# Performance work log

Measured on AMD Instinct MI355X. Metric: run time of the kernel, lower is better.

## Reference

```python
import jax, jax.numpy as jnp
import numpy as np

N = 100_000   # nodes
E = 1_600_000 # edges (avg degree 16)
D = 128       # input_dim
H = 128       # hidden_dim
G = 64        # graphs in batch
C = 2         # num_classes


def setup_inputs() -> dict:
    key = jax.random.key(0)
    ks = jax.random.split(key, 16)
    x = jax.random.normal(ks[0], (N, D), dtype=jnp.float32)
    edge_index = jax.random.randint(ks[1], (2, E), 0, N, dtype=jnp.int32)
    batch = jnp.sort(jax.random.randint(ks[2], (N,), 0, G, dtype=jnp.int32))
    def lin(k, fin, fout):
        s = 1.0 / np.sqrt(fin)
        kw, kb = jax.random.split(k)
        W = jax.random.uniform(kw, (fin, fout), jnp.float32, -s, s)
        b = jax.random.uniform(kb, (fout,), jnp.float32, -s, s)
        return W, b
    W0, b0 = lin(ks[3], D, H)
    W1, b1 = lin(ks[4], H, H)
    W2, b2 = lin(ks[5], H, H)
    Wc1, bc1 = lin(ks[6], 2 * H, H)
    Wc2, bc2 = lin(ks[7], H, C)
    return dict(x=x, edge_index=edge_index, batch=batch,
                W0=W0, b0=b0, W1=W1, b1=b1, W2=W2, b2=b2,
                Wc1=Wc1, bc1=bc1, Wc2=Wc2, bc2=bc2)


def _gcn_layer(x, W, b, src, dst, dinv):
    # GCNConv with self-loops and symmetric normalization:
    # out_i = sum_{j->i} d_j^{-1/2} d_i^{-1/2} (x_j W) + d_i^{-1} (x_i W) + b
    h = x @ W                                   # [N, H]
    coef = dinv[src] * dinv[dst]                # [E]
    agg = jax.ops.segment_sum(h[src] * coef[:, None], dst, num_segments=N)
    return agg + h * (dinv * dinv)[:, None] + b


def reference(x, edge_index, batch, W0, b0, W1, b1, W2, b2, Wc1, bc1, Wc2, bc2):
    src, dst = edge_index[0], edge_index[1]
    # degree with self-loops (in-degree on target nodes + 1)
    deg = jax.ops.segment_sum(jnp.ones((E,), jnp.float32), dst, num_segments=N) + 1.0
    dinv = jax.lax.rsqrt(deg)
    for W, b in ((W0, b0), (W1, b1), (W2, b2)):
        x = jax.nn.relu(_gcn_layer(x, W, b, src, dst, dinv))
        # dropout: inference mode -> identity
    # global mean pool per graph
    sums = jax.ops.segment_sum(x, batch, num_segments=G)            # [G, H]
    cnt = jax.ops.segment_sum(jnp.ones((N,), jnp.float32), batch, num_segments=G)
    pooled = sums / jnp.maximum(cnt, 1.0)[:, None]
    combined = jnp.concatenate([pooled, pooled], axis=1)            # [G, 2H]
    hcls = jax.nn.relu(combined @ Wc1 + bc1)
    return hcls @ Wc2 + bc2                                         # [G, C]
```

## Files before the change

kernel.cpp:

```cpp
#include <hip/hip_runtime.h>

#define HDIM 128
#define GCOUNT 64
#define CHUNK 2048

__device__ __forceinline__ float bfl(unsigned u) { return __uint_as_float(u << 16); }
__device__ __forceinline__ unsigned short f2bf(float f) {
  unsigned u = __float_as_uint(f);
  unsigned r = (u + 0x7fffu + ((u >> 16) & 1u)) >> 16;
  return (unsigned short)r;
}
__device__ __forceinline__ unsigned pk2(float a, float b) {
  return (unsigned)f2bf(a) | ((unsigned)f2bf(b) << 16);
}

typedef __attribute__((ext_vector_type(8))) short short8;
typedef __attribute__((ext_vector_type(4))) float f32x4;

__device__ __forceinline__ unsigned qb(float v, float rinv) {
  int q = (int)rintf(v * rinv);
  return (unsigned)(q & 0xff);
}


__global__ void mega1(const float* __restrict__ W0, const float* __restrict__ W1,
                      const float* __restrict__ W2,
                      unsigned short* __restrict__ h0, unsigned short* __restrict__ l0,
                      unsigned short* __restrict__ h1, unsigned short* __restrict__ l1,
                      unsigned short* __restrict__ h2, unsigned short* __restrict__ l2,
                      float* __restrict__ pooled, float* __restrict__ gcnt, int pz,
                      const int* __restrict__ dst, int E, int G, int NB1,
                      int* __restrict__ gcount,
                      const float* __restrict__ x, uint2* __restrict__ S,
                      uint2* __restrict__ Sb, float* __restrict__ csaP,
                      float* __restrict__ csbP,
                      float* __restrict__ cs_base, int n) {
  __shared__ int hist[512];
  int b = blockIdx.x, t = threadIdx.x;
  if (b < 192) {
    int w = b >> 6;
    int idx = (b & 63) * 256 + t;
    const float* W = (w == 0) ? W0 : (w == 1) ? W1 : W2;
    unsigned short* hi = (w == 0) ? h0 : (w == 1) ? h1 : h2;
    unsigned short* lo = (w == 0) ? l0 : (w == 1) ? l1 : l2;
    int k = idx >> 7, nn = idx & 127;
    float wv = W[idx];
    unsigned short h = f2bf(wv);
    float hf = __uint_as_float((unsigned)h << 16);
    unsigned short l = f2bf(wv - hf);
    int kb = k >> 5, quad = (k >> 3) & 3, e = k & 7;
    int nt = nn >> 4, m = nn & 15;
    int di = (((kb * 8 + nt) * 64) + quad * 16 + m) * 8 + e;
    hi[di] = h;
    lo[di] = l;
  } else if (b < 192 + pz) {
    int i = (b - 192) * 256 + t;
    if (i < GCOUNT * HDIM) pooled[i] = 0.f;
    else if (i - GCOUNT * HDIM < GCOUNT) gcnt[i - GCOUNT * HDIM] = 0.f;
    if (b == 192) {
      if (t < 16) S[(size_t)n * 16 + t] = make_uint2(0u, 0u);
      else if (t < 32) Sb[(size_t)n * 16 + (t - 16)] = make_uint2(0u, 0u);
      else if (t == 32) csaP[n] = 0.f;
      else if (t == 33) csbP[n] = 0.f;
    }
  } else if (b < 192 + pz + G) {
    int blk = b - 192 - pz;
    for (int i = t; i < NB1; i += 256) hist[i] = 0;
    __syncthreads();
    int base = blk * CHUNK;
    #pragma unroll
    for (int j = 0; j < CHUNK / 256; j++) {
      int e = base + j * 256 + t;
      if (e < E) atomicAdd(&hist[dst[e] >> 8], 1);
    }
    __syncthreads();
    for (int i = t; i < NB1; i += 256) gcount[i * G + blk] = hist[i];
  } else {
    int idx = (b - 192 - pz - G) * 16 + (t >> 4);
    int l = t & 15;
    int ridx = min(idx, n - 1);
    float4 f0 = ((const float4*)x)[(size_t)ridx * 32 + l * 2];
    float4 f1 = ((const float4*)x)[(size_t)ridx * 32 + l * 2 + 1];
    float v0 = f0.x, v1 = f0.y, v2 = f0.z, v3 = f0.w;
    float v4 = f1.x, v5 = f1.y, v6 = f1.z, v7 = f1.w;
    float mx = fmaxf(fmaxf(fmaxf(fabsf(v0), fabsf(v1)), fmaxf(fabsf(v2), fabsf(v3))),
                     fmaxf(fmaxf(fabsf(v4), fabsf(v5)), fmaxf(fabsf(v6), fabsf(v7))));
    mx = fmaxf(mx, __shfl_xor(mx, 1));
    mx = fmaxf(mx, __shfl_xor(mx, 2));
    mx = fmaxf(mx, __shfl_xor(mx, 4));
    mx = fmaxf(mx, __shfl_xor(mx, 8));
    float c = mx * (1.0f / 127.0f);
    float rinv = (mx > 0.f) ? 127.0f / mx : 0.f;
    if (idx < n) {
      unsigned lo = qb(v0, rinv) | (qb(v1, rinv) << 8) | (qb(v2, rinv) << 16) | (qb(v3, rinv) << 24);
      unsigned hi = qb(v4, rinv) | (qb(v5, rinv) << 8) | (qb(v6, rinv) << 16) | (qb(v7, rinv) << 24);
      S[(size_t)idx * 16 + l] = make_uint2(lo, hi);
      if (l == 0) cs_base[idx] = c;
    }
  }
}


__global__ void scanA(int* __restrict__ g, int* __restrict__ bsum, int M) {
  __shared__ int sh[1024];
  int t = threadIdx.x;
  int i = blockIdx.x * 1024 + t;
  int v = (i < M) ? g[i] : 0;
  sh[t] = v;
  __syncthreads();
  for (int off = 1; off < 1024; off <<= 1) {
    int u = (t >= off) ? sh[t - off] : 0;
    __syncthreads();
    sh[t] += u;
    __syncthreads();
  }
  if (i < M) g[i] = sh[t] - v;
  if (t == 1023) bsum[blockIdx.x] = sh[1023];
}

__global__ void scanB(int* __restrict__ g, const int* __restrict__ bsum, int nb, int M) {
  __shared__ int sh[512];
  int t = threadIdx.x;
  if (t < 512) sh[t] = (t < nb) ? bsum[t] : 0;
  __syncthreads();
  for (int off = 1; off < 512; off <<= 1) {
    int u = (t < 512 && t >= off) ? sh[t - off] : 0;
    __syncthreads();
    if (t < 512) sh[t] += u;
    __syncthreads();
  }
  #pragma unroll
  for (int k = 0; k < 2; k++) {
    int i = blockIdx.x * 2048 + k * 1024 + t;
    if (i < M) {
      int j = i >> 10;
      if (j) g[i] += sh[j - 1];
    }
  }
}


__global__ void rs_scatter(const int* __restrict__ src, const int* __restrict__ dst,
                           const int* __restrict__ gscan, int E, int G, int NB1,
                           uint2* __restrict__ sp) {
  __shared__ int run[512];
  int blk = blockIdx.x, t = threadIdx.x;
  for (int i = t; i < NB1; i += 256) run[i] = gscan[i * G + blk];
  __syncthreads();
  int base = blk * CHUNK;
  #pragma unroll
  for (int j = 0; j < CHUNK / 256; j++) {
    int e = base + j * 256 + t;
    if (e < E) {
      int d = dst[e];
      int pos = atomicAdd(&run[d >> 8], 1);
      sp[pos] = make_uint2((unsigned)d, (unsigned)src[e]);
    }
  }
}


__global__ void csr_fine(const uint2* __restrict__ sp, const int* __restrict__ gscan,
                         int E, int G, int NB1,
                         int* __restrict__ rowp, int* __restrict__ rowe,
                         int* __restrict__ colv,
                         float* __restrict__ dinv, const float* __restrict__ cs_base,
                         float* __restrict__ cs, int n) {
  __shared__ int hist[256];
  __shared__ int scn[256];
  __shared__ int run2[256];
  int hb = blockIdx.x, t = threadIdx.x;
  int O = gscan[hb * G];
  int Oe = (hb == NB1 - 1) ? E : gscan[(hb + 1) * G];
  int PO = ((O + 3) & ~3) + hb * 1024;
  if (t < 256) hist[t] = 0;
  __syncthreads();
  for (int e = O + t; e < Oe; e += 512) atomicAdd(&hist[sp[e].x & 255], 1);
  __syncthreads();
  int v = 0, pv = 0;
  if (t < 256) { v = hist[t]; pv = (v + 3) & ~3; scn[t] = pv; }
  __syncthreads();
  for (int off = 1; off < 256; off <<= 1) {
    int u = (t < 256 && t >= off) ? scn[t - off] : 0;
    __syncthreads();
    if (t < 256) scn[t] += u;
    __syncthreads();
  }
  if (t < 256) {
    int st = PO + scn[t] - pv;
    run2[t] = st;
    int d = (hb << 8) + t;
    rowp[d] = st;
    rowe[d] = st + pv;
    for (int i = v; i < pv; i++) colv[st + i] = n;
    if (d < n) {
      float dv = rsqrtf((float)v + 1.0f);
      dinv[d] = dv;
      cs[d] = cs_base[d] * dv;
    }
  }
  __syncthreads();
  for (int e = O + t; e < Oe; e += 512) {
    uint2 p = sp[e];
    int pos = atomicAdd(&run2[p.x & 255], 1);
    colv[pos] = (int)p.y;
  }
}


__device__ __forceinline__ void acc8(uint2 v, float c, float* a) {
  int xx = (int)v.x, yy = (int)v.y;
  a[0] += c * (float)(signed char)(xx);
  a[1] += c * (float)(signed char)(xx >> 8);
  a[2] += c * (float)(signed char)(xx >> 16);
  a[3] += c * (float)(xx >> 24);
  a[4] += c * (float)(signed char)(yy);
  a[5] += c * (float)(signed char)(yy >> 8);
  a[6] += c * (float)(signed char)(yy >> 16);
  a[7] += c * (float)(yy >> 24);
}


__device__ __forceinline__ void agg_phase(
    const uint2* __restrict__ S, const float* __restrict__ cs,
    const float* __restrict__ dinv,
    const int* __restrict__ rowp, const int* __restrict__ rowe,
    const int* __restrict__ col,
    uint4* At, int block0, int t, int n) {
  int grp = t >> 4, gl = t & 15;
  #pragma unroll 1
  for (int k = 0; k < 4; k++) {
    int lrow = grp * 4 + k;
    int g = block0 + lrow;
    uint4 o = make_uint4(0u, 0u, 0u, 0u);
    if (g < n) {
      float a[8];
      {
        uint2 q = S[(size_t)g * 16 + gl];
        float c = cs[g];
        int xx = (int)q.x, yy = (int)q.y;
        a[0] = c * (float)(signed char)(xx);
        a[1] = c * (float)(signed char)(xx >> 8);
        a[2] = c * (float)(signed char)(xx >> 16);
        a[3] = c * (float)(xx >> 24);
        a[4] = c * (float)(signed char)(yy);
        a[5] = c * (float)(signed char)(yy >> 8);
        a[6] = c * (float)(signed char)(yy >> 16);
        a[7] = c * (float)(yy >> 24);
      }
      int e = rowp[g], e1 = rowe[g];
      if (e < e1) {
        int4 ca = *(const int4*)(col + e);
        uint2 q0 = S[(size_t)ca.x * 16 + gl];
        uint2 q1 = S[(size_t)ca.y * 16 + gl];
        uint2 q2 = S[(size_t)ca.z * 16 + gl];
        uint2 q3 = S[(size_t)ca.w * 16 + gl];
        float c0 = cs[ca.x], c1 = cs[ca.y], c2 = cs[ca.z], c3 = cs[ca.w];
        #pragma unroll 1
        for (e += 4; e < e1; e += 4) {
          int4 cn = *(const int4*)(col + e);
          uint2 p0 = S[(size_t)cn.x * 16 + gl];
          uint2 p1 = S[(size_t)cn.y * 16 + gl];
          uint2 p2 = S[(size_t)cn.z * 16 + gl];
          uint2 p3 = S[(size_t)cn.w * 16 + gl];
          float d0 = cs[cn.x], d1 = cs[cn.y], d2 = cs[cn.z], d3 = cs[cn.w];
          acc8(q0, c0, a); acc8(q1, c1, a); acc8(q2, c2, a); acc8(q3, c3, a);
          q0 = p0; q1 = p1; q2 = p2; q3 = p3;
          c0 = d0; c1 = d1; c2 = d2; c3 = d3;
        }
        acc8(q0, c0, a); acc8(q1, c1, a); acc8(q2, c2, a); acc8(q3, c3, a);
      }
      float d = dinv[g];
      o.x = pk2(a[0] * d, a[1] * d);
      o.y = pk2(a[2] * d, a[3] * d);
      o.z = pk2(a[4] * d, a[5] * d);
      o.w = pk2(a[6] * d, a[7] * d);
    }
    At[(gl << 6) + (lrow ^ (gl & 7))] = o;
  }
}

__device__ __forceinline__ void stage16(uint4* Wl, const uint4* __restrict__ WT, int t) {
  #pragma unroll
  for (int i = 0; i < 4; i++) {
    int idx = t + i * 256;
    Wl[idx] = WT[idx];
  }
}

__device__ __forceinline__ void mfma2(const uint4* Wl, const uint4* av, f32x4* acc,
                                      int kbase, int lane) {
  #pragma unroll
  for (int kk = 0; kk < 2; kk++) {
    short8 af = __builtin_bit_cast(short8, av[kbase + kk]);
    #pragma unroll
    for (int nt = 0; nt < 8; nt++) {
      uint4 b = Wl[(kk * 8 + nt) * 64 + lane];
      acc[nt] = __builtin_amdgcn_mfma_f32_16x16x32_bf16(af, __builtin_bit_cast(short8, b), acc[nt], 0, 0, 0);
    }
  }
}

__global__ __launch_bounds__(256, 4) void fused_q8(
    const uint2* __restrict__ S, const float* __restrict__ cs,
    const float* __restrict__ dinv,
    const int* __restrict__ rowp, const int* __restrict__ rowe,
    const int* __restrict__ col,
    const uint4* __restrict__ WThi, const uint4* __restrict__ WTlo,
    const float* __restrict__ bias,
    unsigned char* __restrict__ Sout, float* __restrict__ csout, int n) {
  __shared__ __align__(16) char smem[16384];
  uint4* At = (uint4*)smem;
  uint4* Wl = (uint4*)smem;
  int t = threadIdx.x;
  int lane = t & 63, wv = t >> 6;
  int m = lane & 15, quad = lane >> 4;
  int block0 = blockIdx.x * 64;

  agg_phase(S, cs, dinv, rowp, rowe, col, At, block0, t, n);
  __syncthreads();

  uint4 av[4];
  #pragma unroll
  for (int kb = 0; kb < 4; kb++) {
    int glr = kb * 4 + quad;
    av[kb] = At[(glr << 6) + ((wv * 16 + m) ^ (glr & 7))];
  }
  __syncthreads();

  f32x4 acc[8];
  #pragma unroll
  for (int i = 0; i < 8; i++) acc[i] = (f32x4){0.f, 0.f, 0.f, 0.f};

  stage16(Wl, WThi, t);        __syncthreads();
  mfma2(Wl, av, acc, 0, lane); __syncthreads();
  stage16(Wl, WThi + 1024, t); __syncthreads();
  mfma2(Wl, av, acc, 2, lane); __syncthreads();
  stage16(Wl, WTlo, t);        __syncthreads();
  mfma2(Wl, av, acc, 0, lane); __syncthreads();
  stage16(Wl, WTlo + 1024, t); __syncthreads();
  mfma2(Wl, av, acc, 2, lane); __syncthreads();

  char* stg = smem;
  float* LcA = (float*)(smem + 9216);
  #pragma unroll
  for (int r = 0; r < 4; r++) {
    int lrow = wv * 16 + quad * 4 + r;
    int grow = block0 + lrow;
    float sc = (grow < n) ? dinv[grow] : 0.f;
    float v[8];
    float mx = 0.f;
    #pragma unroll
    for (int nt = 0; nt < 8; nt++) {
      v[nt] = fmaxf(acc[nt][r] + bias[nt * 16 + m], 0.f) * sc;
      mx = fmaxf(mx, v[nt]);
    }
    mx = fmaxf(mx, __shfl_xor(mx, 1));
    mx = fmaxf(mx, __shfl_xor(mx, 2));
    mx = fmaxf(mx, __shfl_xor(mx, 4));
    mx = fmaxf(mx, __shfl_xor(mx, 8));
    float c = mx * (1.0f / 127.0f);
    float rinv = (mx > 0.f) ? 127.0f / mx : 0.f;
    #pragma unroll
    for (int nt = 0; nt < 8; nt++) {
      stg[lrow * 144 + nt * 16 + m] = (char)(int)rintf(v[nt] * rinv);
    }
    if (m == 0) LcA[lrow] = c;
  }
  __syncthreads();
  for (int i = t; i < 512; i += 256) {
    int lrow = i >> 3, seg = i & 7;
    int grow = block0 + lrow;
    if (grow < n)
      ((uint4*)Sout)[(size_t)grow * 8 + seg] = *(const uint4*)&stg[lrow * 144 + seg * 16];
  }
  if (t < 64 && block0 + t < n) csout[block0 + t] = LcA[t];
}

__global__ __launch_bounds__(256, 4) void fused_final(
    const uint2* __restrict__ S, const float* __restrict__ cs,
    const float* __restrict__ dinv,
    const int* __restrict__ rowp, const int* __restrict__ rowe,
    const int* __restrict__ col,
    const uint4* __restrict__ WThi, const uint4* __restrict__ WTlo,
    const float* __restrict__ bias, const int* __restrict__ batch,
    float* __restrict__ pooled, float* __restrict__ gcnt, int n) {
  __shared__ __align__(16) char smem[16384];
  uint4* At = (uint4*)smem;
  uint4* Wl = (uint4*)smem;
  int t = threadIdx.x;
  int lane = t & 63, wv = t >> 6;
  int m = lane & 15, quad = lane >> 4;
  int block0 = blockIdx.x * 64;

  agg_phase(S, cs, dinv, rowp, rowe, col, At, block0, t, n);
  __syncthreads();

  uint4 av[4];
  #pragma unroll
  for (int kb = 0; kb < 4; kb++) {
    int glr = kb * 4 + quad;
    av[kb] = At[(glr << 6) + ((wv * 16 + m) ^ (glr & 7))];
  }
  __syncthreads();

  f32x4 acc[8];
  #pragma unroll
  for (int i = 0; i < 8; i++) acc[i] = (f32x4){0.f, 0.f, 0.f, 0.f};

  stage16(Wl, WThi, t);        __syncthreads();
  mfma2(Wl, av, acc, 0, lane); __syncthreads();
  stage16(Wl, WThi + 1024, t); __syncthreads();
  mfma2(Wl, av, acc, 2, lane); __syncthreads();
  stage16(Wl, WTlo, t);        __syncthreads();
  mfma2(Wl, av, acc, 0, lane); __syncthreads();
  stage16(Wl, WTlo + 1024, t); __syncthreads();
  mfma2(Wl, av, acc, 2, lane); __syncthreads();

  unsigned short* Ls = (unsigned short*)smem;
  #pragma unroll
  for (int r = 0; r < 4; r++) {
    int lrow = wv * 16 + quad * 4 + r;
    #pragma unroll
    for (int nt = 0; nt < 8; nt++) {
      float v = fmaxf(acc[nt][r] + bias[nt * 16 + m], 0.f);
      Ls[lrow * 128 + nt * 16 + m] = f2bf(v);
    }
  }
  __syncthreads();
  if (t < 128) {
    float a2 = 0.f, cl = 0.f;
    int gcur = -1;
    for (int r = 0; r < 64; r++) {
      int grow = block0 + r;
      if (grow >= n) break;
      int gr = batch[grow];
      if (gr != gcur) {
        if (gcur >= 0) {
          atomicAdd(&pooled[gcur * HDIM + t], a2);
          if (t == 0) atomicAdd(&gcnt[gcur], cl);
        }
        a2 = 0.f; cl = 0.f; gcur = gr;
      }
      a2 += bfl((unsigned)Ls[r * 128 + t]);
      cl += 1.f;
    }
    if (gcur >= 0) {
      atomicAdd(&pooled[gcur * HDIM + t], a2);
      if (t == 0) atomicAdd(&gcnt[gcur], cl);
    }
  }
}


__global__ void cls_kernel(const float* __restrict__ pooled, const float* __restrict__ gcnt,
                           const float* __restrict__ Wc1, const float* __restrict__ bc1,
                           const float* __restrict__ Wc2, const float* __restrict__ bc2,
                           float* __restrict__ out) {
  __shared__ float p[HDIM];
  __shared__ float r0s[HDIM], r1s[HDIM];
  int g = blockIdx.x, t = threadIdx.x;
  float c = fmaxf(gcnt[g], 1.0f);
  p[t] = pooled[g * HDIM + t] / c;
  __syncthreads();
  float acc = bc1[t];
  for (int k = 0; k < HDIM; k++) {
    acc += p[k] * (Wc1[k * HDIM + t] + Wc1[(HDIM + k) * HDIM + t]);
  }
  float h = fmaxf(acc, 0.f);
  r0s[t] = h * Wc2[t * 2 + 0];
  r1s[t] = h * Wc2[t * 2 + 1];
  __syncthreads();
  for (int s2 = 64; s2 > 0; s2 >>= 1) {
    if (t < s2) { r0s[t] += r0s[t + s2]; r1s[t] += r1s[t + s2]; }
    __syncthreads();
  }
  if (t == 0) {
    out[g * 2 + 0] = r0s[0] + bc2[0];
    out[g * 2 + 1] = r1s[0] + bc2[1];
  }
}


extern "C" void kernel_launch(void* const* d_in, const int* in_sizes, int n_in,
                              void* d_out, int out_size, void* d_ws, size_t ws_size,
                              hipStream_t stream) {
  const float* x   = (const float*)d_in[0];
  const int*   ei  = (const int*)d_in[1];
  const int*   bat = (const int*)d_in[2];
  const float* W0  = (const float*)d_in[3];
  const float* b0  = (const float*)d_in[4];
  const float* W1  = (const float*)d_in[5];
  const float* b1  = (const float*)d_in[6];
  const float* W2  = (const float*)d_in[7];
  const float* b2  = (const float*)d_in[8];
  const float* Wc1 = (const float*)d_in[9];
  const float* bc1 = (const float*)d_in[10];
  const float* Wc2 = (const float*)d_in[11];
  const float* bc2 = (const float*)d_in[12];
  float* out = (float*)d_out;

  int N = in_sizes[0] / HDIM;
  int E = in_sizes[1] / 2;
  const int* src = ei;
  const int* dst = ei + E;

  int NB1 = (N + 255) >> 8;
  int G = (E + CHUNK - 1) / CHUNK;
  int M = NB1 * G;

  char* ws = (char*)d_ws;
  size_t off = 0;
  auto alloc = [&](size_t bytes) -> void* {
    void* p = (void*)(ws + off);
    off += (bytes + 511) & ~(size_t)511;
    return p;
  };
  unsigned char* Sa = (unsigned char*)alloc((size_t)(N + 1) * HDIM * 2);
  unsigned char* Sb = Sa + (size_t)(N + 1) * HDIM;
  float* csa  = (float*)alloc((size_t)(N + 2) * 4);
  float* csb  = (float*)alloc((size_t)(N + 2) * 4);
  float* cs_base = (float*)alloc((size_t)N * 4);
  float* dinv = (float*)alloc((size_t)N * 4);
  int*   rowp = (int*)alloc((size_t)(NB1 * 256 + 2) * 4);
  int*   rowe = (int*)alloc((size_t)(NB1 * 256 + 2) * 4);
  int*   colv = (int*)alloc((size_t)(E + NB1 * 1024 + 1024) * 4);
  uint2* sp   = (uint2*)alloc((size_t)E * 8);
  float* pooled = (float*)alloc((size_t)GCOUNT * HDIM * 4);
  float* gcnt   = (float*)alloc((size_t)GCOUNT * 4);
  unsigned short* wt_hi[3], *wt_lo[3];
  for (int i = 0; i < 3; i++) {
    wt_hi[i] = (unsigned short*)alloc(HDIM * HDIM * 2);
    wt_lo[i] = (unsigned short*)alloc(HDIM * HDIM * 2);
  }
  int* gcount = (int*)alloc((size_t)(M + 2) * 4);
  int nbM = (M + 1023) / 1024;
  int* bsum = (int*)alloc((size_t)nbM * 4);

  int pz = (GCOUNT * HDIM + GCOUNT + 255) / 256;
  int psb = (N + 15) / 16;
  mega1<<<192 + pz + G + psb, 256, 0, stream>>>(W0, W1, W2,
      wt_hi[0], wt_lo[0], wt_hi[1], wt_lo[1], wt_hi[2], wt_lo[2],
      pooled, gcnt, pz, dst, E, G, NB1, gcount,
      x, (uint2*)Sa, (uint2*)Sb, csa, csb, cs_base, N);

  scanA<<<nbM, 1024, 0, stream>>>(gcount, bsum, M);
  scanB<<<(M + 2047) / 2048, 1024, 0, stream>>>(gcount, bsum, nbM, M);

  rs_scatter<<<G, 256, 0, stream>>>(src, dst, gcount, E, G, NB1, sp);
  csr_fine<<<NB1, 512, 0, stream>>>(sp, gcount, E, G, NB1, rowp, rowe, colv,
      dinv, cs_base, csa, N);

  int fusedBlocks = (N + 63) / 64;

  fused_q8<<<fusedBlocks, 256, 0, stream>>>((const uint2*)Sa, csa, dinv, rowp, rowe, colv,
      (const uint4*)wt_hi[0], (const uint4*)wt_lo[0], b0, Sb, csb, N);

  fused_q8<<<fusedBlocks, 256, 0, stream>>>((const uint2*)Sb, csb, dinv, rowp, rowe, colv,
      (const uint4*)wt_hi[1], (const uint4*)wt_lo[1], b1, Sa, csa, N);

  fused_final<<<fusedBlocks, 256, 0, stream>>>((const uint2*)Sa, csa, dinv, rowp, rowe, colv,
      (const uint4*)wt_hi[2], (const uint4*)wt_lo[2], b2, bat, pooled, gcnt, N);

  cls_kernel<<<GCOUNT, HDIM, 0, stream>>>(pooled, gcnt, Wc1, bc1, Wc2, bc2, out);
}
```

Baseline: 328.7 us.

## Pack CSR scatter entries, enlarge chunk, and pipeline edge loads across rows

Packs the scatter intermediate into a single 32-bit word per edge (24-bit source plus the low 8 bits of the destination), halving that buffer's traffic, and doubles CHUNK for the radix scatter. The aggregation now treats each thread group's four rows as one continuous edge stream, so the software-pipelined gather prefetch carries across row boundaries instead of draining and refilling per row. This relies on the padded contiguity of the CSR layout and on node ids fitting in 24 bits. It also adds a scheduling barrier and extra control flow inside the inner loop.

```diff
diff --git a/kernel.cpp b/kernel.cpp
--- a/kernel.cpp
+++ b/kernel.cpp
@@ -2,7 +2,7 @@
 
 #define HDIM 128
 #define GCOUNT 64
-#define CHUNK 2048
+#define CHUNK 4096
 
 __device__ __forceinline__ float bfl(unsigned u) { return __uint_as_float(u << 16); }
 __device__ __forceinline__ unsigned short f2bf(float f) {
@@ -142,7 +142,7 @@
 
 __global__ void rs_scatter(const int* __restrict__ src, const int* __restrict__ dst,
                            const int* __restrict__ gscan, int E, int G, int NB1,
-                           uint2* __restrict__ sp) {
+                           unsigned* __restrict__ sp) {
   __shared__ int run[512];
   int blk = blockIdx.x, t = threadIdx.x;
   for (int i = t; i < NB1; i += 256) run[i] = gscan[i * G + blk];
@@ -154,13 +154,13 @@
     if (e < E) {
       int d = dst[e];
       int pos = atomicAdd(&run[d >> 8], 1);
-      sp[pos] = make_uint2((unsigned)d, (unsigned)src[e]);
-    }
-  }
-}
-
-
-__global__ void csr_fine(const uint2* __restrict__ sp, const int* __restrict__ gscan,
+      sp[pos] = (unsigned)src[e] | ((unsigned)(d & 255) << 24);
+    }
+  }
+}
+
+
+__global__ void csr_fine(const unsigned* __restrict__ sp, const int* __restrict__ gscan,
                          int E, int G, int NB1,
                          int* __restrict__ rowp, int* __restrict__ rowe,
                          int* __restrict__ colv,
@@ -175,7 +175,7 @@
   int PO = ((O + 3) & ~3) + hb * 1024;
   if (t < 256) hist[t] = 0;
   __syncthreads();
-  for (int e = O + t; e < Oe; e += 512) atomicAdd(&hist[sp[e].x & 255], 1);
+  for (int e = O + t; e < Oe; e += 512) atomicAdd(&hist[sp[e] >> 24], 1);
   __syncthreads();
   int v = 0, pv = 0;
   if (t < 256) { v = hist[t]; pv = (v + 3) & ~3; scn[t] = pv; }
@@ -201,9 +201,9 @@
   }
   __syncthreads();
   for (int e = O + t; e < Oe; e += 512) {
-    uint2 p = sp[e];
-    int pos = atomicAdd(&run2[p.x & 255], 1);
-    colv[pos] = (int)p.y;
+    unsigned p = sp[e];
+    int pos = atomicAdd(&run2[p >> 24], 1);
+    colv[pos] = (int)(p & 0xFFFFFFu);
   }
 }
 
@@ -228,55 +228,80 @@
     const int* __restrict__ col,
     uint4* At, int block0, int t, int n) {
   int grp = t >> 4, gl = t & 15;
-  #pragma unroll 1
-  for (int k = 0; k < 4; k++) {
-    int lrow = grp * 4 + k;
-    int g = block0 + lrow;
+  int g0 = block0 + grp * 4;
+
+  float a[8];
+  int r = 0;
+
+  auto initRow = [&](int g) {
+    if (g < n) {
+      uint2 q = S[(size_t)g * 16 + gl];
+      float c = cs[g];
+      int xx = (int)q.x, yy = (int)q.y;
+      a[0] = c * (float)(signed char)(xx);
+      a[1] = c * (float)(signed char)(xx >> 8);
+      a[2] = c * (float)(signed char)(xx >> 16);
+      a[3] = c * (float)(xx >> 24);
+      a[4] = c * (float)(signed char)(yy);
+      a[5] = c * (float)(signed char)(yy >> 8);
+      a[6] = c * (float)(signed char)(yy >> 16);
+      a[7] = c * (float)(yy >> 24);
+    } else {
+      #pragma unroll
+      for (int i = 0; i < 8; i++) a[i] = 0.f;
+    }
+  };
+  auto finRow = [&](int rr) {
+    int g = g0 + rr;
     uint4 o = make_uint4(0u, 0u, 0u, 0u);
     if (g < n) {
-      float a[8];
-      {
-        uint2 q = S[(size_t)g * 16 + gl];
-        float c = cs[g];
-        int xx = (int)q.x, yy = (int)q.y;
-        a[0] = c * (float)(signed char)(xx);
-        a[1] = c * (float)(signed char)(xx >> 8);
-        a[2] = c * (float)(signed char)(xx >> 16);
-        a[3] = c * (float)(xx >> 24);
-        a[4] = c * (float)(signed char)(yy);
-        a[5] = c * (float)(signed char)(yy >> 8);
-        a[6] = c * (float)(signed char)(yy >> 16);
-        a[7] = c * (float)(yy >> 24);
-      }
-      int e = rowp[g], e1 = rowe[g];
-      if (e < e1) {
-        int4 ca = *(const int4*)(col + e);
-        uint2 q0 = S[(size_t)ca.x * 16 + gl];
-        uint2 q1 = S[(size_t)ca.y * 16 + gl];
-        uint2 q2 = S[(size_t)ca.z * 16 + gl];
-        uint2 q3 = S[(size_t)ca.w * 16 + gl];
-        float c0 = cs[ca.x], c1 = cs[ca.y], c2 = cs[ca.z], c3 = cs[ca.w];
-        #pragma unroll 1
-        for (e += 4; e < e1; e += 4) {
-          int4 cn = *(const int4*)(col + e);
-          uint2 p0 = S[(size_t)cn.x * 16 + gl];
-          uint2 p1 = S[(size_t)cn.y * 16 + gl];
-          uint2 p2 = S[(size_t)cn.z * 16 + gl];
-          uint2 p3 = S[(size_t)cn.w * 16 + gl];
-          float d0 = cs[cn.x], d1 = cs[cn.y], d2 = cs[cn.z], d3 = cs[cn.w];
-          acc8(q0, c0, a); acc8(q1, c1, a); acc8(q2, c2, a); acc8(q3, c3, a);
-          q0 = p0; q1 = p1; q2 = p2; q3 = p3;
-          c0 = d0; c1 = d1; c2 = d2; c3 = d3;
-        }
-        acc8(q0, c0, a); acc8(q1, c1, a); acc8(q2, c2, a); acc8(q3, c3, a);
-      }
       float d = dinv[g];
       o.x = pk2(a[0] * d, a[1] * d);
       o.y = pk2(a[2] * d, a[3] * d);
       o.z = pk2(a[4] * d, a[5] * d);
       o.w = pk2(a[6] * d, a[7] * d);
     }
+    int lrow = grp * 4 + rr;
     At[(gl << 6) + (lrow ^ (gl & 7))] = o;
+  };
+
+  initRow(g0);
+  int cur = rowp[g0];
+  int stop = rowe[g0];
+  int eEnd = rowe[g0 + 3];
+
+  while (cur >= stop && r < 3) { finRow(r); r++; initRow(g0 + r); stop = rowe[g0 + r]; }
+
+  if (cur < eEnd) {
+    int4 ca = *(const int4*)(col + cur);
+    uint2 q0 = S[(size_t)ca.x * 16 + gl];
+    uint2 q1 = S[(size_t)ca.y * 16 + gl];
+    uint2 q2 = S[(size_t)ca.z * 16 + gl];
+    uint2 q3 = S[(size_t)ca.w * 16 + gl];
+    float c0 = cs[ca.x], c1 = cs[ca.y], c2 = cs[ca.z], c3 = cs[ca.w];
+    #pragma unroll 1
+    for (int e = cur + 4; e < eEnd; e += 4) {
+      int4 cn = *(const int4*)(col + e);
+      uint2 p0 = S[(size_t)cn.x * 16 + gl];
+      uint2 p1 = S[(size_t)cn.y * 16 + gl];
+      uint2 p2 = S[(size_t)cn.z * 16 + gl];
+      uint2 p3 = S[(size_t)cn.w * 16 + gl];
+      float d0 = cs[cn.x], d1 = cs[cn.y], d2 = cs[cn.z], d3 = cs[cn.w];
+      __builtin_amdgcn_sched_barrier(0);
+      acc8(q0, c0, a); acc8(q1, c1, a); acc8(q2, c2, a); acc8(q3, c3, a);
+      cur += 4;
+      while (cur >= stop && r < 3) { finRow(r); r++; initRow(g0 + r); stop = rowe[g0 + r]; }
+      q0 = p0; q1 = p1; q2 = p2; q3 = p3;
+      c0 = d0; c1 = d1; c2 = d2; c3 = d3;
+    }
+    acc8(q0, c0, a); acc8(q1, c1, a); acc8(q2, c2, a); acc8(q3, c3, a);
+  }
+  for (;;) {
+    finRow(r);
+    r++;
+    if (r >= 4) break;
+    initRow(g0 + r);
+    stop = rowe[g0 + r];
   }
 }
 
@@ -525,7 +550,7 @@
   int*   rowp = (int*)alloc((size_t)(NB1 * 256 + 2) * 4);
   int*   rowe = (int*)alloc((size_t)(NB1 * 256 + 2) * 4);
   int*   colv = (int*)alloc((size_t)(E + NB1 * 1024 + 1024) * 4);
-  uint2* sp   = (uint2*)alloc((size_t)E * 8);
+  unsigned* sp = (unsigned*)alloc((size_t)E * 4);
   float* pooled = (float*)alloc((size_t)GCOUNT * HDIM * 4);
   float* gcnt   = (float*)alloc((size_t)GCOUNT * 4);
   unsigned short* wt_hi[3], *wt_lo[3];
```

New measurement: 343.0 us. +4.3%, slower.

## Fold scanB into scatter kernels, pack edge pairs into 32 bits, interleave row bounds

Applied to the files above, without the earlier changes.

Drops the scanB kernel: rs_scatter and csr_fine each redo the small block-sum scan in shared memory and add the offset when they read gcount. Scatter records shrink from 8 bytes to 4 by packing the source index with the low 8 bits of the destination in the top byte. rowp and rowe are merged into one int2 array, so the aggregation reads one 8-byte load per row. The aim is to save a launch and cut traffic during CSR construction, at the cost of redundant scans per block and packing that assumes node ids fit in 24 bits.

```diff
diff --git a/kernel.cpp b/kernel.cpp
--- a/kernel.cpp
+++ b/kernel.cpp
@@ -118,64 +118,74 @@
   if (t == 1023) bsum[blockIdx.x] = sh[1023];
 }
 
-__global__ void scanB(int* __restrict__ g, const int* __restrict__ bsum, int nb, int M) {
-  __shared__ int sh[512];
-  int t = threadIdx.x;
-  if (t < 512) sh[t] = (t < nb) ? bsum[t] : 0;
+
+__global__ void rs_scatter(const int* __restrict__ src, const int* __restrict__ dst,
+                           const int* __restrict__ gscan, const int* __restrict__ bsum,
+                           int nb, int E, int G, int NB1,
+                           unsigned* __restrict__ sp) {
+  __shared__ int run[512];
+  __shared__ int sb[512];
+  int blk = blockIdx.x, t = threadIdx.x;
+  sb[t] = (t < nb) ? bsum[t] : 0;
   __syncthreads();
   for (int off = 1; off < 512; off <<= 1) {
-    int u = (t < 512 && t >= off) ? sh[t - off] : 0;
-    __syncthreads();
-    if (t < 512) sh[t] += u;
-    __syncthreads();
-  }
-  #pragma unroll
-  for (int k = 0; k < 2; k++) {
-    int i = blockIdx.x * 2048 + k * 1024 + t;
-    if (i < M) {
-      int j = i >> 10;
-      if (j) g[i] += sh[j - 1];
-    }
-  }
-}
-
-
-__global__ void rs_scatter(const int* __restrict__ src, const int* __restrict__ dst,
-                           const int* __restrict__ gscan, int E, int G, int NB1,
-                           uint2* __restrict__ sp) {
-  __shared__ int run[512];
-  int blk = blockIdx.x, t = threadIdx.x;
-  for (int i = t; i < NB1; i += 256) run[i] = gscan[i * G + blk];
+    int u = (t >= off) ? sb[t - off] : 0;
+    __syncthreads();
+    sb[t] += u;
+    __syncthreads();
+  }
+  for (int i = t; i < NB1; i += 512) {
+    int idx = i * G + blk;
+    int j = idx >> 10;
+    run[i] = gscan[idx] + (j ? sb[j - 1] : 0);
+  }
   __syncthreads();
   int base = blk * CHUNK;
   #pragma unroll
-  for (int j = 0; j < CHUNK / 256; j++) {
-    int e = base + j * 256 + t;
+  for (int j = 0; j < CHUNK / 512; j++) {
+    int e = base + j * 512 + t;
     if (e < E) {
       int d = dst[e];
       int pos = atomicAdd(&run[d >> 8], 1);
-      sp[pos] = make_uint2((unsigned)d, (unsigned)src[e]);
-    }
-  }
-}
-
-
-__global__ void csr_fine(const uint2* __restrict__ sp, const int* __restrict__ gscan,
+      sp[pos] = (unsigned)src[e] | ((unsigned)(d & 255) << 24);
+    }
+  }
+}
+
+
+__global__ void csr_fine(const unsigned* __restrict__ sp, const int* __restrict__ gscan,
+                         const int* __restrict__ bsum, int nb,
                          int E, int G, int NB1,
-                         int* __restrict__ rowp, int* __restrict__ rowe,
-                         int* __restrict__ colv,
+                         int2* __restrict__ rowpe, int* __restrict__ colv,
                          float* __restrict__ dinv, const float* __restrict__ cs_base,
                          float* __restrict__ cs, int n) {
+  __shared__ int sb[512];
   __shared__ int hist[256];
   __shared__ int scn[256];
   __shared__ int run2[256];
   int hb = blockIdx.x, t = threadIdx.x;
-  int O = gscan[hb * G];
-  int Oe = (hb == NB1 - 1) ? E : gscan[(hb + 1) * G];
+  sb[t] = (t < nb) ? bsum[t] : 0;
+  __syncthreads();
+  for (int off = 1; off < 512; off <<= 1) {
+    int u = (t >= off) ? sb[t - off] : 0;
+    __syncthreads();
+    sb[t] += u;
+    __syncthreads();
+  }
+  int iO = hb * G;
+  int jO = iO >> 10;
+  int O = gscan[iO] + (jO ? sb[jO - 1] : 0);
+  int Oe;
+  if (hb == NB1 - 1) Oe = E;
+  else {
+    int i2 = (hb + 1) * G;
+    int j2 = i2 >> 10;
+    Oe = gscan[i2] + (j2 ? sb[j2 - 1] : 0);
+  }
   int PO = ((O + 3) & ~3) + hb * 1024;
   if (t < 256) hist[t] = 0;
   __syncthreads();
-  for (int e = O + t; e < Oe; e += 512) atomicAdd(&hist[sp[e].x & 255], 1);
+  for (int e = O + t; e < Oe; e += 512) atomicAdd(&hist[sp[e] >> 24], 1);
   __syncthreads();
   int v = 0, pv = 0;
   if (t < 256) { v = hist[t]; pv = (v + 3) & ~3; scn[t] = pv; }
@@ -190,8 +200,7 @@
     int st = PO + scn[t] - pv;
     run2[t] = st;
     int d = (hb << 8) + t;
-    rowp[d] = st;
-    rowe[d] = st + pv;
+    rowpe[d] = make_int2(st, st + pv);
     for (int i = v; i < pv; i++) colv[st + i] = n;
     if (d < n) {
       float dv = rsqrtf((float)v + 1.0f);
@@ -201,9 +210,9 @@
   }
   __syncthreads();
   for (int e = O + t; e < Oe; e += 512) {
-    uint2 p = sp[e];
-    int pos = atomicAdd(&run2[p.x & 255], 1);
-    colv[pos] = (int)p.y;
+    unsigned p = sp[e];
+    int pos = atomicAdd(&run2[p >> 24], 1);
+    colv[pos] = (int)(p & 0xFFFFFFu);
   }
 }
 
@@ -224,7 +233,7 @@
 __device__ __forceinline__ void agg_phase(
     const uint2* __restrict__ S, const float* __restrict__ cs,
     const float* __restrict__ dinv,
-    const int* __restrict__ rowp, const int* __restrict__ rowe,
+    const int2* __restrict__ rowpe,
     const int* __restrict__ col,
     uint4* At, int block0, int t, int n) {
   int grp = t >> 4, gl = t & 15;
@@ -248,7 +257,8 @@
         a[6] = c * (float)(signed char)(yy >> 16);
         a[7] = c * (float)(yy >> 24);
       }
-      int e = rowp[g], e1 = rowe[g];
+      int2 pe = rowpe[g];
+      int e = pe.x, e1 = pe.y;
       if (e < e1) {
         int4 ca = *(const int4*)(col + e);
         uint2 q0 = S[(size_t)ca.x * 16 + gl];
@@ -304,7 +314,7 @@
 __global__ __launch_bounds__(256, 4) void fused_q8(
     const uint2* __restrict__ S, const float* __restrict__ cs,
     const float* __restrict__ dinv,
-    const int* __restrict__ rowp, const int* __restrict__ rowe,
+    const int2* __restrict__ rowpe,
     const int* __restrict__ col,
     const uint4* __restrict__ WThi, const uint4* __restrict__ WTlo,
     const float* __restrict__ bias,
@@ -317,7 +327,7 @@
   int m = lane & 15, quad = lane >> 4;
   int block0 = blockIdx.x * 64;
 
-  agg_phase(S, cs, dinv, rowp, rowe, col, At, block0, t, n);
+  agg_phase(S, cs, dinv, rowpe, col, At, block0, t, n);
   __syncthreads();
 
   uint4 av[4];
@@ -380,7 +390,7 @@
 __global__ __launch_bounds__(256, 4) void fused_final(
     const uint2* __restrict__ S, const float* __restrict__ cs,
     const float* __restrict__ dinv,
-    const int* __restrict__ rowp, const int* __restrict__ rowe,
+    const int2* __restrict__ rowpe,
     const int* __restrict__ col,
     const uint4* __restrict__ WThi, const uint4* __restrict__ WTlo,
     const float* __restrict__ bias, const int* __restrict__ batch,
@@ -393,7 +403,7 @@
   int m = lane & 15, quad = lane >> 4;
   int block0 = blockIdx.x * 64;
 
-  agg_phase(S, cs, dinv, rowp, rowe, col, At, block0, t, n);
+  agg_phase(S, cs, dinv, rowpe, col, At, block0, t, n);
   __syncthreads();
 
   uint4 av[4];
@@ -522,10 +532,9 @@
   float* csb  = (float*)alloc((size_t)(N + 2) * 4);
   float* cs_base = (float*)alloc((size_t)N * 4);
   float* dinv = (float*)alloc((size_t)N * 4);
-  int*   rowp = (int*)alloc((size_t)(NB1 * 256 + 2) * 4);
-  int*   rowe = (int*)alloc((size_t)(NB1 * 256 + 2) * 4);
+  int2*  rowpe = (int2*)alloc((size_t)(NB1 * 256 + 2) * 8);
   int*   colv = (int*)alloc((size_t)(E + NB1 * 1024 + 1024) * 4);
-  uint2* sp   = (uint2*)alloc((size_t)E * 8);
+  unsigned* sp = (unsigned*)alloc((size_t)E * 4);
   float* pooled = (float*)alloc((size_t)GCOUNT * HDIM * 4);
   float* gcnt   = (float*)alloc((size_t)GCOUNT * 4);
   unsigned short* wt_hi[3], *wt_lo[3];
@@ -545,21 +554,20 @@
       x, (uint2*)Sa, (uint2*)Sb, csa, csb, cs_base, N);
 
   scanA<<<nbM, 1024, 0, stream>>>(gcount, bsum, M);
-  scanB<<<(M + 2047) / 2048, 1024, 0, stream>>>(gcount, bsum, nbM, M);
-
-  rs_scatter<<<G, 256, 0, stream>>>(src, dst, gcount, E, G, NB1, sp);
-  csr_fine<<<NB1, 512, 0, stream>>>(sp, gcount, E, G, NB1, rowp, rowe, colv,
+
+  rs_scatter<<<G, 512, 0, stream>>>(src, dst, gcount, bsum, nbM, E, G, NB1, sp);
+  csr_fine<<<NB1, 512, 0, stream>>>(sp, gcount, bsum, nbM, E, G, NB1, rowpe, colv,
       dinv, cs_base, csa, N);
 
   int fusedBlocks = (N + 63) / 64;
 
-  fused_q8<<<fusedBlocks, 256, 0, stream>>>((const uint2*)Sa, csa, dinv, rowp, rowe, colv,
+  fused_q8<<<fusedBlocks, 256, 0, stream>>>((const uint2*)Sa, csa, dinv, rowpe, colv,
       (const uint4*)wt_hi[0], (const uint4*)wt_lo[0], b0, Sb, csb, N);
 
-  fused_q8<<<fusedBlocks, 256, 0, stream>>>((const uint2*)Sb, csb, dinv, rowp, rowe, colv,
+  fused_q8<<<fusedBlocks, 256, 0, stream>>>((const uint2*)Sb, csb, dinv, rowpe, colv,
       (const uint4*)wt_hi[1], (const uint4*)wt_lo[1], b1, Sa, csa, N);
 
-  fused_final<<<fusedBlocks, 256, 0, stream>>>((const uint2*)Sa, csa, dinv, rowp, rowe, colv,
+  fused_final<<<fusedBlocks, 256, 0, stream>>>((const uint2*)Sa, csa, dinv, rowpe, colv,
       (const uint4*)wt_hi[2], (const uint4*)wt_lo[2], b2, bat, pooled, gcnt, N);
 
   cls_kernel<<<GCOUNT, HDIM, 0, stream>>>(pooled, gcnt, Wc1, bc1, Wc2, bc2, out);
```

New measurement: 318.1 us (median of 3 runs). 1.03x faster.
